# Optimization experiments

Measured on AMD Instinct MI355X. Metric: run time of the kernel, lower is better.

The kernel has to match this reference:

```python
import jax, jax.numpy as jnp
import numpy as np
import math

TOKEN_DIM = 1024
NUM_HEADS = 16
HEAD_DIM = TOKEN_DIM // NUM_HEADS
T, B, N = 32, 32, 64


def setup_inputs() -> dict:
    key = jax.random.key(0)
    ks = jax.random.split(key, 9)
    query_vec = jax.random.normal(ks[0], (T, B, TOKEN_DIM), dtype=jnp.float32)
    tokens = jax.random.normal(ks[1], (T, B, N, TOKEN_DIM), dtype=jnp.float32)
    gate_logits = jax.random.normal(ks[2], (T, B, N), dtype=jnp.float32)
    scale = 1.0 / math.sqrt(TOKEN_DIM)
    Wq = jax.random.normal(ks[3], (TOKEN_DIM, TOKEN_DIM), dtype=jnp.float32) * scale
    Wk = jax.random.normal(ks[4], (TOKEN_DIM, TOKEN_DIM), dtype=jnp.float32) * scale
    Wv = jax.random.normal(ks[5], (TOKEN_DIM, TOKEN_DIM), dtype=jnp.float32) * scale
    bq = jnp.zeros((TOKEN_DIM,), dtype=jnp.float32)
    bk = jnp.zeros((TOKEN_DIM,), dtype=jnp.float32)
    bv = jnp.zeros((TOKEN_DIM,), dtype=jnp.float32)
    return {"query_vec": query_vec, "tokens": tokens, "gate_logits": gate_logits,
            "Wq": Wq, "bq": bq, "Wk": Wk, "bk": bk, "Wv": Wv, "bv": bv}


def reference(query_vec, tokens, gate_logits, Wq, bq, Wk, bk, Wv, bv):
    # QKV projections
    q = query_vec @ Wq + bq                      # [T,B,D]
    k = tokens @ Wk + bk                         # [T,B,N,D]
    v = tokens @ Wv + bv                         # [T,B,N,D]
    q = q.reshape(T, B, NUM_HEADS, HEAD_DIM)
    k = k.reshape(T, B, N, NUM_HEADS, HEAD_DIM)
    v = v.reshape(T, B, N, NUM_HEADS, HEAD_DIM)
    logits = jnp.einsum('tbhd,tbnhd->tbhn', q, k) / math.sqrt(HEAD_DIM)
    logits = logits + gate_logits[:, :, None, :]
    attn = jax.nn.softmax(logits, axis=-1)       # [T,B,H,N]
    attended = jnp.einsum('tbhn,tbnhd->tbhd', attn, v)
    attended = attended.reshape(T, B, TOKEN_DIM)
    mean_attn = attn.mean(axis=2)                # [T,B,N]
    return (attended, mean_attn, logits)
```

## Files before the change

### kernel.cpp

```cpp
#include <hip/hip_runtime.h>
#include <hip/hip_bf16.h>

typedef __attribute__((ext_vector_type(4))) float f32x4;
typedef __attribute__((ext_vector_type(8))) short bf16x8;
typedef unsigned int u32;
typedef unsigned short u16;

#define DEV static __device__ __forceinline__


DEV u16 f2bf(float x){
  union { float f; u32 u; } v; v.f = x;
  u32 r = v.u + 0x7FFFu + ((v.u >> 16) & 1u);
  return (u16)(r >> 16);
}
DEV float bf2f(u16 s){
  union { u32 u; float f; } v; v.u = ((u32)s) << 16;
  return v.f;
}

#define MFMA16(a,b,c) __builtin_amdgcn_mfma_f32_16x16x32_bf16((a),(b),(c),0,0,0)

#define SWZ(n) ((((n)&3)<<5) | ((((n)>>2)&1)<<4))

DEV void bar_lgkm(){
  __builtin_amdgcn_sched_barrier(0);
  asm volatile("s_waitcnt lgkmcnt(0)" ::: "memory");
  __builtin_amdgcn_s_barrier();
  __builtin_amdgcn_sched_barrier(0);
}
DEV void bar_full(){
  __builtin_amdgcn_sched_barrier(0);
  asm volatile("s_waitcnt vmcnt(0) lgkmcnt(0)" ::: "memory");
  __builtin_amdgcn_s_barrier();
  __builtin_amdgcn_sched_barrier(0);
}

DEV bf16x8 cvt8(f32x4 lo, f32x4 hi){
  union { u32 u[4]; bf16x8 v; } r;
  asm("v_cvt_pk_bf16_f32 %0, %1, %2" : "=v"(r.u[0]) : "v"(lo.x), "v"(lo.y));
  asm("v_cvt_pk_bf16_f32 %0, %1, %2" : "=v"(r.u[1]) : "v"(lo.z), "v"(lo.w));
  asm("v_cvt_pk_bf16_f32 %0, %1, %2" : "=v"(r.u[2]) : "v"(hi.x), "v"(hi.y));
  asm("v_cvt_pk_bf16_f32 %0, %1, %2" : "=v"(r.u[3]) : "v"(hi.z), "v"(hi.w));
  return r.v;
}

DEV void stage8(const float* __restrict__ tokens, int tbn, int tk0,
                char* smem, int bb, int w, int l){
  char* ldsb = smem + (size_t)bb*32768 + (size_t)w*8192;
  const char* gb = (const char*)tokens + (size_t)tbn*262144 + (size_t)tk0*4096;
  #pragma unroll
  for (int j = 0; j < 8; ++j){
    const int nloc  = w*2 + (j >> 2);
    const int inner = (((j & 3)*1024) + l*16) ^ SWZ(nloc);
    __builtin_amdgcn_global_load_lds(
        (const __attribute__((address_space(1))) u32*)(gb + (size_t)nloc*4096 + inner),
        (__attribute__((address_space(3))) u32*)(ldsb + j*1024),
        16, 0, 0);
  }
}

__global__ __launch_bounds__(256) void k_convert(
    const float* __restrict__ Wq, const float* __restrict__ Wk, const float* __restrict__ Wv,
    u16* __restrict__ WqT, u16* __restrict__ WkB, u16* __restrict__ WvT){
  __shared__ u16 tile[64][65];
  const int which = blockIdx.y;
  const float* src = which==0 ? Wq : (which==1 ? Wk : Wv);
  const int bi = (blockIdx.x >> 4) << 6;
  const int bj = (blockIdx.x & 15) << 6;
  const int t  = threadIdx.x;
  #pragma unroll
  for (int k2 = 0; k2 < 16; ++k2){
    int e = t + (k2 << 8);
    int r = e >> 6, c = e & 63;
    tile[r][c] = f2bf(src[(size_t)(bi + r)*1024 + bj + c]);
  }
  __syncthreads();
  if (which == 1){
    #pragma unroll
    for (int k2 = 0; k2 < 16; ++k2){
      int e = t + (k2 << 8); int r = e >> 6, c = e & 63;
      WkB[(size_t)(bi + r)*1024 + bj + c] = tile[r][c];
    }
  } else {
    u16* dst = which==0 ? WqT : WvT;
    #pragma unroll
    for (int k2 = 0; k2 < 16; ++k2){
      int e = t + (k2 << 8); int r = e >> 6, c = e & 63;
      dst[(size_t)(bj + r)*1024 + bi + c] = tile[c][r];
    }
  }
}

__global__ __launch_bounds__(256) void k_qproj(
    const float* __restrict__ qv, const u16* __restrict__ WqT, const float* __restrict__ bq,
    float* __restrict__ qf, u16* __restrict__ qb){
  const int l = threadIdx.x & 63, w = threadIdx.x >> 6;
  const int wm = w & 1, wn = w >> 1;
  const int g = l >> 4, li = l & 15;
  const int m_base = blockIdx.x*64 + wm*32;
  const int n_base = blockIdx.y*64 + wn*32;
  f32x4 acc[2][2];
  #pragma unroll
  for (int i=0;i<2;++i)
    #pragma unroll
    for (int j=0;j<2;++j) acc[i][j] = (f32x4)0.0f;

  #pragma unroll 4
  for (int kb = 0; kb < 32; ++kb){
    const int k0 = kb*32 + g*8;
    bf16x8 a[2], b[2];
    #pragma unroll
    for (int rt = 0; rt < 2; ++rt){
      const float* p = qv + (size_t)(m_base + rt*16 + li)*1024 + k0;
      f32x4 lo = *(const f32x4*)p;
      f32x4 hi = *(const f32x4*)(p+4);
      union { u16 s[8]; bf16x8 v; } u;
      u.s[0]=f2bf(lo.x); u.s[1]=f2bf(lo.y); u.s[2]=f2bf(lo.z); u.s[3]=f2bf(lo.w);
      u.s[4]=f2bf(hi.x); u.s[5]=f2bf(hi.y); u.s[6]=f2bf(hi.z); u.s[7]=f2bf(hi.w);
      a[rt] = u.v;
    }
    #pragma unroll
    for (int ct = 0; ct < 2; ++ct)
      b[ct] = *(const bf16x8*)(WqT + (size_t)(n_base + ct*16 + li)*1024 + k0);
    #pragma unroll
    for (int rt = 0; rt < 2; ++rt)
      #pragma unroll
      for (int ct = 0; ct < 2; ++ct)
        acc[rt][ct] = MFMA16(a[rt], b[ct], acc[rt][ct]);
  }
  #pragma unroll
  for (int rt=0;rt<2;++rt)
    #pragma unroll
    for (int ct=0;ct<2;++ct)
      #pragma unroll
      for (int r=0;r<4;++r){
        int m = m_base + rt*16 + g*4 + r;
        int n = n_base + ct*16 + li;
        float val = acc[rt][ct][r] + bq[n];
        qf[(size_t)m*1024 + n] = val;
        qb[(size_t)m*1024 + n] = f2bf(val);
      }
}

__global__ __launch_bounds__(256) void k_umat(
    const u16* __restrict__ qb, const u16* __restrict__ WkB, u16* __restrict__ U){
  __shared__ __align__(16) u16 stile[64][64];
  const int l = threadIdx.x & 63, w = threadIdx.x >> 6;
  const int wm = w & 1, wn = w >> 1, g = l >> 4, li = l & 15;
  const int tb0 = blockIdx.x*64, d0 = blockIdx.y*64, h = blockIdx.z;
  f32x4 acc[2][2];
  #pragma unroll
  for (int i=0;i<2;++i)
    #pragma unroll
    for (int j=0;j<2;++j) acc[i][j] = (f32x4)0.0f;

  #pragma unroll
  for (int kb = 0; kb < 2; ++kb){
    const int k0 = h*64 + kb*32 + g*8;
    bf16x8 a[2], b[2];
    #pragma unroll
    for (int rt=0;rt<2;++rt)
      a[rt] = *(const bf16x8*)(qb + (size_t)(tb0 + wm*32 + rt*16 + li)*1024 + k0);
    #pragma unroll
    for (int ct=0;ct<2;++ct)
      b[ct] = *(const bf16x8*)(WkB + (size_t)(d0 + wn*32 + ct*16 + li)*1024 + k0);
    #pragma unroll
    for (int rt=0;rt<2;++rt)
      #pragma unroll
      for (int ct=0;ct<2;++ct)
        acc[rt][ct] = MFMA16(a[rt], b[ct], acc[rt][ct]);
  }
  #pragma unroll
  for (int rt=0;rt<2;++rt)
    #pragma unroll
    for (int ct=0;ct<2;++ct)
      #pragma unroll
      for (int r=0;r<4;++r)
        stile[wm*32 + rt*16 + g*4 + r][wn*32 + ct*16 + li] = f2bf(acc[rt][ct][r]);
  __syncthreads();
  const int r = threadIdx.x >> 2, cg4 = threadIdx.x & 3;
  f32x4* dst = (f32x4*)(U + ((size_t)(tb0 + r)*16 + h)*1024 + d0 + cg4*16);
  const f32x4* s4 = (const f32x4*)(&stile[r][cg4*16]);
  dst[0] = s4[0]; dst[1] = s4[1];
}

#define K3_LDS 65536
__global__ __launch_bounds__(256, 2) void k_attn(
    const float* __restrict__ tokens, const float* __restrict__ gate,
    const u16* __restrict__ U, const float* __restrict__ qf, const float* __restrict__ bk,
    float* __restrict__ out_logits, float* __restrict__ out_mean, u16* __restrict__ ctx){
  extern __shared__ __align__(16) char smem[];
  __shared__ __align__(16) char sstat[8960];
  float* part_s   = (float*)(sstat);
  float* logits_s = (float*)(sstat + 4096);
  float* p_s      = (float*)(sstat + 8192);
  float* csum     = (float*)(sstat + 8704);
  float* r_s      = (float*)(sstat + 8768);
  float* mzs      = (float*)(sstat + 8832);
  const int tb = blockIdx.x;
  const int tid = threadIdx.x;
  const int l = tid & 63, w = tid >> 6, g = l >> 4, li = l & 15;
  const int sh = tid >> 4, sj = tid & 15;

  bf16x8 a[8];
  const bf16x8* Ub = (const bf16x8*)(U + (size_t)tb*16384);
  #pragma unroll
  for (int i = 0; i < 8; ++i)
    a[i] = Ub[li*128 + (w*8 + i)*4 + g];

  {
    const float* qp = qf + (size_t)tb*1024 + sh*64 + sj*4;
    const float* bp = bk + sh*64 + sj*4;
    float part = qp[0]*bp[0] + qp[1]*bp[1] + qp[2]*bp[2] + qp[3]*bp[3];
    part += __shfl_xor(part, 1); part += __shfl_xor(part, 2);
    part += __shfl_xor(part, 4); part += __shfl_xor(part, 8);
    if (sj == 0) csum[sh] = part;
  }

  float m_run = -1e30f, z_run = 0.0f;
  f32x4 cacc[4][4];
  #pragma unroll
  for (int i=0;i<4;++i)
    #pragma unroll
    for (int j=0;j<4;++j) cacc[i][j] = (f32x4)0.0f;

  stage8(tokens, tb, 0, smem, 0, w, l);

  for (int r = 0; r < 8; ++r){
    const int n0 = r*8;
    char* bufc = smem + (size_t)(r & 1)*32768;

    bar_full();
    if (r + 1 < 8)
      stage8(tokens, tb, (r+1)*8, smem, (r+1) & 1, w, l);

    {
      const int row = li & 7;
      const int sw  = SWZ(row);
      f32x4 acc = (f32x4)0.0f;
      #pragma unroll
      for (int i = 0; i < 8; ++i){
        const int p0b = (w*8 + i)*128 + g*32;
        f32x4 lo = *(const f32x4*)(bufc + row*4096 + ((p0b     ) ^ sw));
        f32x4 hi = *(const f32x4*)(bufc + row*4096 + ((p0b + 16) ^ sw));
        acc = MFMA16(a[i], cvt8(lo, hi), acc);
      }
      *(f32x4*)(part_s + (size_t)(w*64 + l)*4) = acc;
    }
    bar_lgkm();

    if (sj < 8){
      const int idx = ((sh >> 2)*16 + sj)*4 + (sh & 3);
      float lv = part_s[idx] + part_s[256 + idx] + part_s[512 + idx] + part_s[768 + idx];
      lv = (lv + csum[sh])*0.125f + gate[(size_t)tb*64 + n0 + sj];
      logits_s[sh*64 + n0 + sj] = lv;
      out_logits[(size_t)tb*1024 + sh*64 + n0 + sj] = lv;
      float cm = lv;
      cm = fmaxf(cm, __shfl_xor(cm, 1));
      cm = fmaxf(cm, __shfl_xor(cm, 2));
      cm = fmaxf(cm, __shfl_xor(cm, 4));
      float m_new = fmaxf(m_run, cm);
      float rsc = __expf(m_run - m_new);
      float p0 = __expf(lv - m_new);
      float zs = p0;
      zs += __shfl_xor(zs, 1); zs += __shfl_xor(zs, 2); zs += __shfl_xor(zs, 4);
      z_run = z_run * rsc + zs;
      m_run = m_new;
      p_s[sj*16 + sh] = p0;
      if (sj == 0){
        r_s[sh] = rsc;
        if (r == 7){ mzs[sh*2] = m_new; mzs[sh*2 + 1] = 1.0f / z_run; }
      }
    }
    bar_lgkm();

    {
      float rr4[4];
      #pragma unroll
      for (int hh = 0; hh < 4; ++hh) rr4[hh] = r_s[w*4 + hh];
      #pragma unroll
      for (int dq = 0; dq < 4; ++dq)
        #pragma unroll
        for (int hh = 0; hh < 4; ++hh) cacc[dq][hh] *= rr4[hh];
      #pragma unroll
      for (int nl = 0; nl < 8; ++nl){
        const f32x4 p = *(const f32x4*)(p_s + nl*16 + w*4);
        const int swn = SWZ(nl);
        #pragma unroll
        for (int dq = 0; dq < 4; ++dq){
          const f32x4 t = *(const f32x4*)(bufc + (size_t)nl*4096 + ((dq*1024 + l*16) ^ swn));
          #pragma unroll
          for (int hh = 0; hh < 4; ++hh)
            cacc[dq][hh] += t * p[hh];
        }
      }
    }
  }

  if (tid < 64){
    float s = 0.0f;
    #pragma unroll
    for (int h = 0; h < 16; ++h)
      s += __expf(logits_s[h*64 + tid] - mzs[h*2]) * mzs[h*2 + 1];
    out_mean[(size_t)tb*64 + tid] = s * 0.0625f;
  }
  #pragma unroll
  for (int hh = 0; hh < 4; ++hh){
    const int h = w*4 + hh;
    const float zinv = mzs[h*2 + 1];
    #pragma unroll
    for (int dq = 0; dq < 4; ++dq){
      f32x4 v = cacc[dq][hh];
      uint2 pk;
      pk.x = (u32)f2bf(v.x * zinv) | ((u32)f2bf(v.y * zinv) << 16);
      pk.y = (u32)f2bf(v.z * zinv) | ((u32)f2bf(v.w * zinv) << 16);
      *(uint2*)(ctx + ((size_t)tb*16 + h)*1024 + dq*256 + l*4) = pk;
    }
  }
}

__global__ __launch_bounds__(256) void k_attended(
    const u16* __restrict__ ctx, const u16* __restrict__ WvT, const float* __restrict__ bv,
    float* __restrict__ out_att){
  const int l = threadIdx.x & 63, w = threadIdx.x >> 6;
  const int wm = w & 1, wn = w >> 1, g = l >> 4, li = l & 15;
  const int tb0 = blockIdx.x*64, h = blockIdx.y;
  f32x4 acc[2][2];
  #pragma unroll
  for (int i=0;i<2;++i)
    #pragma unroll
    for (int j=0;j<2;++j) acc[i][j] = (f32x4)0.0f;

  #pragma unroll 4
  for (int kb = 0; kb < 32; ++kb){
    const int k0 = kb*32 + g*8;
    bf16x8 a[2], b[2];
    #pragma unroll
    for (int rt=0;rt<2;++rt)
      a[rt] = *(const bf16x8*)(ctx + ((size_t)(tb0 + wm*32 + rt*16 + li)*16 + h)*1024 + k0);
    #pragma unroll
    for (int ct=0;ct<2;++ct)
      b[ct] = *(const bf16x8*)(WvT + (size_t)(h*64 + wn*32 + ct*16 + li)*1024 + k0);
    #pragma unroll
    for (int rt=0;rt<2;++rt)
      #pragma unroll
      for (int ct=0;ct<2;++ct)
        acc[rt][ct] = MFMA16(a[rt], b[ct], acc[rt][ct]);
  }
  #pragma unroll
  for (int rt=0;rt<2;++rt)
    #pragma unroll
    for (int ct=0;ct<2;++ct)
      #pragma unroll
      for (int r=0;r<4;++r){
        int m = tb0 + wm*32 + rt*16 + g*4 + r;
        int dout = h*64 + wn*32 + ct*16 + li;
        out_att[(size_t)m*1024 + dout] = acc[rt][ct][r] + bv[dout];
      }
}

extern "C" void kernel_launch(void* const* d_in, const int* in_sizes, int n_in,
                              void* d_out, int out_size, void* d_ws, size_t ws_size,
                              hipStream_t stream){
  const float* qv     = (const float*)d_in[0];
  const float* tokens = (const float*)d_in[1];
  const float* gate   = (const float*)d_in[2];
  const float* Wq     = (const float*)d_in[3];
  const float* bq     = (const float*)d_in[4];
  const float* Wk     = (const float*)d_in[5];
  const float* bk     = (const float*)d_in[6];
  const float* Wv     = (const float*)d_in[7];
  const float* bv     = (const float*)d_in[8];

  char* ws = (char*)d_ws;
  u16*   WqT = (u16*)(ws);
  u16*   WkB = (u16*)(ws + (2u<<20));
  u16*   WvT = (u16*)(ws + (4u<<20));
  float* qf  = (float*)(ws + (6u<<20));
  u16*   qb  = (u16*)(ws + (10u<<20));
  u16*   U   = (u16*)(ws + (12u<<20));
  u16*   ctxb= (u16*)(ws + (44u<<20));

  float* out_att    = (float*)d_out;
  float* out_mean   = out_att + 1048576;
  float* out_logits = out_att + 1114112;

  (void)hipFuncSetAttribute((const void*)k_attn,
                            hipFuncAttributeMaxDynamicSharedMemorySize, K3_LDS);
  k_convert <<<dim3(256, 3),    256, 0,      stream>>>(Wq, Wk, Wv, WqT, WkB, WvT);
  k_qproj   <<<dim3(16, 16),    256, 0,      stream>>>(qv, WqT, bq, qf, qb);
  k_umat    <<<dim3(16, 16, 16),256, 0,      stream>>>(qb, WkB, U);
  k_attn    <<<dim3(1024),      256, K3_LDS, stream>>>(tokens, gate, U, qf, bk,
                                                       out_logits, out_mean, ctxb);
  k_attended<<<dim3(16, 16),    256, 0,      stream>>>(ctxb, WvT, bv, out_att);
}
```

Before: 160.2 us.

## Make per-wave softmax self-contained and drop a block barrier per chunk

Each wave now computes the logits and online-softmax statistics for its own four heads, instead of a subset of threads doing it for all heads. Because each wave produces the data it consumes, the block-wide barrier per token chunk can go. The rescale factors are shared with a wave shuffle instead of through LDS. Gate values are preloaded into LDS once, and the logits output is written at the end as one coalesced vector store. The cost is that the reduction is duplicated across lanes, with a little extra LDS and a final barrier.

```diff
diff --git a/kernel.cpp b/kernel.cpp
--- a/kernel.cpp
+++ b/kernel.cpp
@@ -191,13 +191,13 @@
     const u16* __restrict__ U, const float* __restrict__ qf, const float* __restrict__ bk,
     float* __restrict__ out_logits, float* __restrict__ out_mean, u16* __restrict__ ctx){
   extern __shared__ __align__(16) char smem[];
-  __shared__ __align__(16) char sstat[8960];
+  __shared__ __align__(16) char sstat[9152];
   float* part_s   = (float*)(sstat);
   float* logits_s = (float*)(sstat + 4096);
   float* p_s      = (float*)(sstat + 8192);
   float* csum     = (float*)(sstat + 8704);
-  float* r_s      = (float*)(sstat + 8768);
-  float* mzs      = (float*)(sstat + 8832);
+  float* gate_s   = (float*)(sstat + 8768);
+  float* mzs      = (float*)(sstat + 9024);
   const int tb = blockIdx.x;
   const int tid = threadIdx.x;
   const int l = tid & 63, w = tid >> 6, g = l >> 4, li = l & 15;
@@ -209,6 +209,7 @@
   for (int i = 0; i < 8; ++i)
     a[i] = Ub[li*128 + (w*8 + i)*4 + g];
 
+  if (tid < 64) gate_s[tid] = gate[(size_t)tb*64 + tid];
   {
     const float* qp = qf + (size_t)tb*1024 + sh*64 + sj*4;
     const float* bp = bk + sh*64 + sj*4;
@@ -218,6 +219,10 @@
     if (sj == 0) csum[sh] = part;
   }
 
+  const int hl  = (l >> 3) & 3;
+  const int hme = w*4 + hl;
+  const int nme = l & 7;
+
   float m_run = -1e30f, z_run = 0.0f;
   f32x4 cacc[4][4];
   #pragma unroll
@@ -250,35 +255,32 @@
     }
     bar_lgkm();
 
-    if (sj < 8){
-      const int idx = ((sh >> 2)*16 + sj)*4 + (sh & 3);
-      float lv = part_s[idx] + part_s[256 + idx] + part_s[512 + idx] + part_s[768 + idx];
-      lv = (lv + csum[sh])*0.125f + gate[(size_t)tb*64 + n0 + sj];
-      logits_s[sh*64 + n0 + sj] = lv;
-      out_logits[(size_t)tb*1024 + sh*64 + n0 + sj] = lv;
+    float rsc;
+    {
+      const int base = w*64 + nme*4 + (hme & 3);
+      float lv = part_s[base] + part_s[256 + base] + part_s[512 + base] + part_s[768 + base];
+      lv = (lv + csum[hme])*0.125f + gate_s[n0 + nme];
       float cm = lv;
       cm = fmaxf(cm, __shfl_xor(cm, 1));
       cm = fmaxf(cm, __shfl_xor(cm, 2));
       cm = fmaxf(cm, __shfl_xor(cm, 4));
       float m_new = fmaxf(m_run, cm);
-      float rsc = __expf(m_run - m_new);
+      rsc = __expf(m_run - m_new);
       float p0 = __expf(lv - m_new);
       float zs = p0;
       zs += __shfl_xor(zs, 1); zs += __shfl_xor(zs, 2); zs += __shfl_xor(zs, 4);
       z_run = z_run * rsc + zs;
       m_run = m_new;
-      p_s[sj*16 + sh] = p0;
-      if (sj == 0){
-        r_s[sh] = rsc;
-        if (r == 7){ mzs[sh*2] = m_new; mzs[sh*2 + 1] = 1.0f / z_run; }
+      if (l < 32){
+        p_s[nme*16 + hme] = p0;
+        logits_s[hme*64 + n0 + nme] = lv;
       }
     }
-    bar_lgkm();
 
     {
       float rr4[4];
       #pragma unroll
-      for (int hh = 0; hh < 4; ++hh) rr4[hh] = r_s[w*4 + hh];
+      for (int hh = 0; hh < 4; ++hh) rr4[hh] = __shfl(rsc, hh*8);
       #pragma unroll
       for (int dq = 0; dq < 4; ++dq)
         #pragma unroll
@@ -298,6 +300,16 @@
     }
   }
 
+  if (l < 32 && (l & 7) == 0){
+    mzs[hme*2]     = m_run;
+    mzs[hme*2 + 1] = 1.0f / z_run;
+  }
+  bar_lgkm();
+
+  {
+    f32x4 v = *(const f32x4*)(logits_s + tid*4);
+    *(f32x4*)(out_logits + (size_t)tb*1024 + tid*4) = v;
+  }
   if (tid < 64){
     float s = 0.0f;
     #pragma unroll
```

After: 159.9 us (median of 2 runs). No clear change (-0.2%).
